# Optimization experiments

Hardware: AMD Instinct MI355X
Metric: run time of the kernel (lower is better)

Reference implementation:

```python
import jax, jax.numpy as jnp
import numpy as np

B, Q, K, A, H, C, O = 32, 512, 512, 256, 8, 32, 256  # batch, queries, keys, channels, heads, head_dim, out_dim


def setup_inputs() -> dict:
    key = jax.random.key(0)
    ks = jax.random.split(key, 12)
    s = 0.02
    return {
        "q_data": jax.random.normal(ks[0], (B, Q, A), jnp.float32),
        "m_data": jax.random.normal(ks[1], (B, K, A), jnp.float32),
        "bias": jax.random.normal(ks[2], (B, 1, 1, K), jnp.float32),
        "nonbatched_bias": jax.random.normal(ks[3], (H, Q, K), jnp.float32),
        "batched_bias": jax.random.normal(ks[4], (B, H, Q, K), jnp.float32),
        "query_w": jax.random.normal(ks[5], (A, H, C), jnp.float32) * s,
        "key_w": jax.random.normal(ks[6], (A, H, C), jnp.float32) * s,
        "value_w": jax.random.normal(ks[7], (A, H, C), jnp.float32) * s,
        "gating_w": jax.random.normal(ks[8], (A, H, C), jnp.float32) * s,
        "gating_b": jnp.ones((H, C), jnp.float32),
        "output_w": jax.random.normal(ks[9], (H, C, O), jnp.float32) * s,
        "output_b": jnp.zeros((O,), jnp.float32),
    }


def reference(q_data, m_data, bias, nonbatched_bias, batched_bias,
              query_w, key_w, value_w, gating_w, gating_b, output_w, output_b):
    key_scale = query_w.shape[-1] ** -0.5
    q = jnp.einsum('bqa,ahc->bqhc', q_data, query_w) * key_scale
    k = jnp.einsum('bka,ahc->bkhc', m_data, key_w)
    v = jnp.einsum('bka,ahc->bkhc', m_data, value_w)
    logits = jnp.einsum('bqhc,bkhc->bhqk', q, k) + bias
    logits = logits + nonbatched_bias[None] + batched_bias
    weights = jax.nn.softmax(logits, axis=-1)
    weighted_avg = jnp.einsum('bhqk,bkhc->bqhc', weights, v)
    gate = jax.nn.sigmoid(jnp.einsum('bqc,chv->bqhv', q_data, gating_w) + gating_b)
    weighted_avg = weighted_avg * gate
    return jnp.einsum('bqhc,hco->bqo', weighted_avg, output_w) + output_b
```

## Files before the change

### kernel.cpp

```cpp
#include <hip/hip_runtime.h>
#include <cstdint>
#include <cstddef>


typedef __attribute__((ext_vector_type(8))) short short8;
typedef __attribute__((ext_vector_type(4))) float f32x4;
typedef __attribute__((ext_vector_type(4))) unsigned int u32x4;
typedef __attribute__((ext_vector_type(2))) unsigned int u32x2;

#define DEVFN static __device__ __forceinline__
#define L2E 1.4426950408889634f

DEVFN float b2f(unsigned int bits16) {
  return __builtin_bit_cast(float, bits16 << 16);
}
DEVFN unsigned int pack2(float a, float b) {
  unsigned int r;
  asm("v_cvt_pk_bf16_f32 %0, %1, %2" : "=v"(r) : "v"(a), "v"(b));
  return r;
}
DEVFN f32x4 mfma16(short8 a, short8 b, f32x4 c) {
  return __builtin_amdgcn_mfma_f32_16x16x32_bf16(a, b, c, 0, 0, 0);
}

__global__ __launch_bounds__(256) void wtrans_kernel(
    const float* __restrict__ qw, const float* __restrict__ kw,
    const float* __restrict__ vw, const float* __restrict__ gw,
    const float* __restrict__ ow,
    unsigned short* __restrict__ wtq, unsigned short* __restrict__ wtk,
    unsigned short* __restrict__ wtv, unsigned short* __restrict__ wtg,
    unsigned short* __restrict__ wt3)
{
  const int matid = blockIdx.x >> 4;
  const int tile  = blockIdx.x & 15;
  const float* src = (matid == 0) ? qw : (matid == 1) ? kw : (matid == 2) ? vw
                   : (matid == 3) ? gw : ow;
  unsigned short* dst = (matid == 0) ? wtq : (matid == 1) ? wtk : (matid == 2) ? wtv
                      : (matid == 3) ? wtg : wt3;
  const int tr = (tile >> 2) * 64, tc = (tile & 3) * 64;
  __shared__ unsigned short T[64 * 72];
  const int t = threadIdx.x;
  {
    const int row = t >> 2, cb = (t & 3) * 16;
#pragma unroll
    for (int ii = 0; ii < 4; ++ii) {
      f32x4 v = *(const f32x4*)&src[(size_t)(tr + row) * 256 + tc + cb + ii * 4];
      u32x2 p; p.x = pack2(v.x, v.y); p.y = pack2(v.z, v.w);
      *(u32x2*)&T[row * 72 + cb + ii * 4] = p;
    }
  }
  __syncthreads();
  {
    const int c0 = t >> 2, rb = (t & 3) * 16;
    unsigned short vals[16];
#pragma unroll
    for (int m = 0; m < 16; ++m) vals[m] = T[(rb + m) * 72 + c0];
    u32x4 s0, s1;
    s0.x = (unsigned)vals[0]  | ((unsigned)vals[1]  << 16);
    s0.y = (unsigned)vals[2]  | ((unsigned)vals[3]  << 16);
    s0.z = (unsigned)vals[4]  | ((unsigned)vals[5]  << 16);
    s0.w = (unsigned)vals[6]  | ((unsigned)vals[7]  << 16);
    s1.x = (unsigned)vals[8]  | ((unsigned)vals[9]  << 16);
    s1.y = (unsigned)vals[10] | ((unsigned)vals[11] << 16);
    s1.z = (unsigned)vals[12] | ((unsigned)vals[13] << 16);
    s1.w = (unsigned)vals[14] | ((unsigned)vals[15] << 16);
    unsigned short* dp = &dst[(size_t)(tc + c0) * 256 + tr + rb];
    *(u32x4*)dp = s0;
    *(u32x4*)(dp + 8) = s1;
  }
}

__global__ __launch_bounds__(512, 4) void proj_kernel(
    const float* __restrict__ q_data, const float* __restrict__ m_data,
    const unsigned short* __restrict__ wtq, const unsigned short* __restrict__ wtk,
    const unsigned short* __restrict__ wtv, const unsigned short* __restrict__ wtg,
    const float* __restrict__ gating_b,
    unsigned short* __restrict__ qp, unsigned short* __restrict__ kp,
    unsigned short* __restrict__ vp, unsigned short* __restrict__ gate)
{
  const int bid = blockIdx.x;
  const bool mside = bid >= 256;
  const int r0 = (mside ? bid - 256 : bid) * 64;
  const float* inp = mside ? m_data : q_data;
  __shared__ unsigned short Alds[64 * 264];
  __shared__ unsigned short Wlds[2][256 * 40];
  const int t = threadIdx.x;
  const int lane = t & 63, wave = t >> 6;
  const int l15 = lane & 15, g = lane >> 4;
  const int stripe = wave & 3, nhalf = wave >> 2;

  {
    const int row = t >> 3, cb = (t & 7) * 32;
    const float* ip = &inp[(size_t)(r0 + row) * 256 + cb];
#pragma unroll
    for (int i = 0; i < 4; ++i) {
      f32x4 a0 = *(const f32x4*)&ip[i * 8];
      f32x4 a1 = *(const f32x4*)&ip[i * 8 + 4];
      u32x4 pk;
      pk.x = pack2(a0.x, a0.y); pk.y = pack2(a0.z, a0.w);
      pk.z = pack2(a1.x, a1.y); pk.w = pack2(a1.z, a1.w);
      *(u32x4*)&Alds[row * 264 + cb + i * 8] = pk;
    }
  }

  const unsigned short* wt0 = mside ? wtk : wtq;
  const unsigned short* wt1 = mside ? wtv : wtg;
  const int wrow = t & 255, whalf = t >> 8;

  {
    const u32x4* wsrc = (const u32x4*)&wt0[(size_t)wrow * 256 + whalf * 16];
    u32x4 a = wsrc[0], b = wsrc[1];
    *(u32x4*)&Wlds[0][wrow * 40 + whalf * 16 + 0] = a;
    *(u32x4*)&Wlds[0][wrow * 40 + whalf * 16 + 8] = b;
  }

  f32x4 acc[8];
#pragma unroll
  for (int j = 0; j < 8; ++j) acc[j] = f32x4{0.f, 0.f, 0.f, 0.f};

  const int arow = (stripe * 16 + l15) * 264 + 8 * g;
  const int grow = r0 + stripe * 16 + l15;
  const int ob = grow >> 9, oq = grow & 511;

#pragma unroll
  for (int s = 0; s < 16; ++s) {
    const int p = s & 1;
    __syncthreads();
    u32x4 nw0, nw1;
    if (s < 15) {
      const unsigned short* wt = (s + 1 < 8) ? wt0 : wt1;
      const u32x4* wsrc =
          (const u32x4*)&wt[(size_t)wrow * 256 + ((s + 1) & 7) * 32 + whalf * 16];
      nw0 = wsrc[0]; nw1 = wsrc[1];
    }
    const int ks = s & 7;
    short8 bf = __builtin_bit_cast(short8, *(const u32x4*)&Alds[arow + ks * 32]);
#pragma unroll
    for (int j = 0; j < 8; ++j) {
      short8 wf = __builtin_bit_cast(short8,
          *(const u32x4*)&Wlds[p][((nhalf * 8 + j) * 16 + l15) * 40 + 8 * g]);
      acc[j] = mfma16(wf, bf, acc[j]);
    }
    if (s < 15) {
      *(u32x4*)&Wlds[p ^ 1][wrow * 40 + whalf * 16 + 0] = nw0;
      *(u32x4*)&Wlds[p ^ 1][wrow * 40 + whalf * 16 + 8] = nw1;
    }
    if (s == 7 || s == 15) {
      const int oi = s >> 3;
      const float QS = 0.17677669529663687f * 1.4426950408889634f;
#pragma unroll
      for (int j = 0; j < 8; ++j) {
        const int n0 = (nhalf * 8 + j) * 16 + 4 * g;
        const int h = n0 >> 5, c0 = n0 & 31;
        const size_t idx = ((size_t)(ob * 8 + h) * 512 + oq) * 32 + c0;
        f32x4 v = acc[j];
        if (!mside) {
          if (oi == 0) {
            u32x2 st;
            st.x = pack2(v.x * QS, v.y * QS);
            st.y = pack2(v.z * QS, v.w * QS);
            *(u32x2*)&qp[idx] = st;
          } else {
            f32x4 gb = *(const f32x4*)&gating_b[n0];
            f32x4 gv;
            gv.x = 1.0f / (1.0f + exp2f(-(v.x + gb.x) * L2E));
            gv.y = 1.0f / (1.0f + exp2f(-(v.y + gb.y) * L2E));
            gv.z = 1.0f / (1.0f + exp2f(-(v.z + gb.z) * L2E));
            gv.w = 1.0f / (1.0f + exp2f(-(v.w + gb.w) * L2E));
            u32x2 st;
            st.x = pack2(gv.x, gv.y); st.y = pack2(gv.z, gv.w);
            *(u32x2*)&gate[idx] = st;
          }
        } else {
          u32x2 st;
          st.x = pack2(v.x, v.y); st.y = pack2(v.z, v.w);
          if (oi == 0) *(u32x2*)&kp[idx] = st;
          else         *(u32x2*)&vp[idx] = st;
        }
        acc[j] = f32x4{0.f, 0.f, 0.f, 0.f};
      }
    }
  }
}

__global__ __launch_bounds__(512, 4) void attn_kernel(
    const unsigned short* __restrict__ qp, const unsigned short* __restrict__ kp,
    const unsigned short* __restrict__ vp,
    const float* __restrict__ bias, const float* __restrict__ nbias,
    const float* __restrict__ bbias,
    unsigned short* __restrict__ wa)
{
  const int bid = blockIdx.x;
  const int h = bid & 7;
  const int qh = (bid >> 3) & 1;
  const int b = bid >> 4;
  const int bh = b * 8 + h;
  const int t = threadIdx.x;
  const int lane = t & 63, wave = t >> 6;
  const int l15 = lane & 15, g = lane >> 4;

  __shared__ unsigned short Klds[512 * 40];
  __shared__ unsigned short Vt[32 * 520];
  __shared__ float Bk[512];

  {
    const int row = t;
    const u32x4* ks = (const u32x4*)&kp[((size_t)bh * 512 + row) * 32];
    u32x4 k0 = ks[0], k1 = ks[1], k2 = ks[2], k3 = ks[3];
    *(u32x4*)&Klds[row * 40 + 0]  = k0;
    *(u32x4*)&Klds[row * 40 + 8]  = k1;
    *(u32x4*)&Klds[row * 40 + 16] = k2;
    *(u32x4*)&Klds[row * 40 + 24] = k3;
    const u32x4* vs = (const u32x4*)&vp[((size_t)bh * 512 + row) * 32];
#pragma unroll
    for (int cc = 0; cc < 4; ++cc) {
      u32x4 vv = vs[cc];
      unsigned int dw0 = vv.x, dw1 = vv.y, dw2 = vv.z, dw3 = vv.w;
      const int c = cc * 8;
      Vt[(c + 0) * 520 + row] = (unsigned short)(dw0 & 0xffff);
      Vt[(c + 1) * 520 + row] = (unsigned short)(dw0 >> 16);
      Vt[(c + 2) * 520 + row] = (unsigned short)(dw1 & 0xffff);
      Vt[(c + 3) * 520 + row] = (unsigned short)(dw1 >> 16);
      Vt[(c + 4) * 520 + row] = (unsigned short)(dw2 & 0xffff);
      Vt[(c + 5) * 520 + row] = (unsigned short)(dw2 >> 16);
      Vt[(c + 6) * 520 + row] = (unsigned short)(dw3 & 0xffff);
      Vt[(c + 7) * 520 + row] = (unsigned short)(dw3 >> 16);
    }
    if (t < 128) {
      f32x4 bv = *(const f32x4*)&bias[(size_t)b * 512 + t * 4];
      bv.x *= L2E; bv.y *= L2E; bv.z *= L2E; bv.w *= L2E;
      *(f32x4*)&Bk[t * 4] = bv;
    }
  }

  const int qbase = qh * 256 + wave * 32;
  short8 qf[2];
#pragma unroll
  for (int qt = 0; qt < 2; ++qt)
    qf[qt] = __builtin_bit_cast(short8,
        *(const u32x4*)&qp[((size_t)bh * 512 + qbase + qt * 16 + l15) * 32 + 8 * g]);

  const float* b0p = bbias + (size_t)bh * 512 * 512 + (size_t)(qbase + l15) * 512 + 4 * g;
  const float* b1p = b0p + 16 * 512;
  const float* n0p = nbias + (size_t)h * 512 * 512 + (size_t)(qbase + l15) * 512 + 4 * g;
  const float* n1p = n0p + 16 * 512;

  f32x4 acc[2][2];
#pragma unroll
  for (int ct = 0; ct < 2; ++ct)
#pragma unroll
    for (int qt = 0; qt < 2; ++qt) acc[ct][qt] = f32x4{0.f, 0.f, 0.f, 0.f};
  float l_part[2] = {0.f, 0.f};

  f32x4 Abb0 = *(const f32x4*)(b0p);
  f32x4 Abb1 = *(const f32x4*)(b0p + 16);
  f32x4 Anb0 = *(const f32x4*)(n0p);
  f32x4 Anb1 = *(const f32x4*)(n0p + 16);

  __syncthreads();

  const int pib = ((g & 1) << 4) | ((g >> 1) << 3);
  const bool godd = (g & 1) != 0;

  for (int kt = 0; kt < 16; ++kt) {
    const int k0 = kt * 32;
    short8 kf0 = __builtin_bit_cast(short8, *(const u32x4*)&Klds[(k0 + l15) * 40 + 8 * g]);
    short8 kf1 = __builtin_bit_cast(short8, *(const u32x4*)&Klds[(k0 + 16 + l15) * 40 + 8 * g]);
    short8 vf0 = __builtin_bit_cast(short8, *(const u32x4*)&Vt[l15 * 520 + k0 + pib]);
    short8 vf1 = __builtin_bit_cast(short8, *(const u32x4*)&Vt[(16 + l15) * 520 + k0 + pib]);
    f32x4 bks0 = *(const f32x4*)&Bk[k0 + 4 * g];
    f32x4 bks1 = *(const f32x4*)&Bk[k0 + 16 + 4 * g];
    f32x4 Bbb0 = *(const f32x4*)(b1p + k0);
    f32x4 Bbb1 = *(const f32x4*)(b1p + k0 + 16);
    f32x4 Bnb0 = *(const f32x4*)(n1p + k0);
    f32x4 Bnb1 = *(const f32x4*)(n1p + k0 + 16);

#pragma unroll
    for (int qt = 0; qt < 2; ++qt) {
      f32x4 bb0, bb1, nb0, nb1;
      if (qt == 0) { bb0 = Abb0; bb1 = Abb1; nb0 = Anb0; nb1 = Anb1; }
      else         { bb0 = Bbb0; bb1 = Bbb1; nb0 = Bnb0; nb1 = Bnb1; }
      f32x4 c0 = bb0 * L2E + (nb0 * L2E + bks0);
      f32x4 c1 = bb1 * L2E + (nb1 * L2E + bks1);
      f32x4 s0 = mfma16(kf0, qf[qt], c0);
      f32x4 s1 = mfma16(kf1, qf[qt], c1);
      if (qt == 0 && kt < 15) {
        Abb0 = *(const f32x4*)(b0p + k0 + 32);
        Abb1 = *(const f32x4*)(b0p + k0 + 48);
        Anb0 = *(const f32x4*)(n0p + k0 + 32);
        Anb1 = *(const f32x4*)(n0p + k0 + 48);
      }
      f32x4 p0, p1;
      p0.x = exp2f(s0.x); p0.y = exp2f(s0.y);
      p0.z = exp2f(s0.z); p0.w = exp2f(s0.w);
      p1.x = exp2f(s1.x); p1.y = exp2f(s1.y);
      p1.z = exp2f(s1.z); p1.w = exp2f(s1.w);
      l_part[qt] += ((p0.x + p0.y) + (p0.z + p0.w)) +
                    ((p1.x + p1.y) + (p1.z + p1.w));
      unsigned int d0 = pack2(p0.x, p0.y), d1 = pack2(p0.z, p0.w);
      unsigned int e0 = pack2(p1.x, p1.y), e1 = pack2(p1.z, p1.w);
      unsigned int pd0 = __shfl_xor(d0, 16, 64), pd1 = __shfl_xor(d1, 16, 64);
      unsigned int pe0 = __shfl_xor(e0, 16, 64), pe1 = __shfl_xor(e1, 16, 64);
      u32x4 pfu;
      pfu.x = godd ? pe0 : d0;
      pfu.y = godd ? pe1 : d1;
      pfu.z = godd ? e0 : pd0;
      pfu.w = godd ? e1 : pd1;
      short8 pf = __builtin_bit_cast(short8, pfu);
      acc[0][qt] = mfma16(vf0, pf, acc[0][qt]);
      acc[1][qt] = mfma16(vf1, pf, acc[1][qt]);
    }
  }

  unsigned short* wab = wa + (size_t)bh * 512 * 32;
#pragma unroll
  for (int qt = 0; qt < 2; ++qt) {
    float l = l_part[qt];
    l += __shfl_xor(l, 16, 64);
    l += __shfl_xor(l, 32, 64);
    const float rl = 1.0f / l;
    const int q = qbase + qt * 16 + l15;
#pragma unroll
    for (int ct = 0; ct < 2; ++ct) {
      f32x4 v = acc[ct][qt];
      u32x2 st;
      st.x = pack2(v.x * rl, v.y * rl);
      st.y = pack2(v.z * rl, v.w * rl);
      *(u32x2*)&wab[q * 32 + ct * 16 + 4 * g] = st;
    }
  }
}

__global__ __launch_bounds__(256, 2) void outp_kernel(
    const unsigned short* __restrict__ wa, const unsigned short* __restrict__ gate,
    const unsigned short* __restrict__ wt3, const float* __restrict__ out_b,
    float* __restrict__ out)
{
  const int r0 = blockIdx.x * 32;
  const int t = threadIdx.x;
  const int lane = t & 63, wave = t >> 6;
  const int l15 = lane & 15, g = lane >> 4;
  const int stripe = wave & 1, half = wave >> 1;
  __shared__ unsigned short Wlds[2][256 * 40];

  const int grow = r0 + stripe * 16 + l15;
  const int b = grow >> 9, q = grow & 511;

  {
    const u32x4* wsrc = (const u32x4*)&wt3[(size_t)t * 256];
    u32x4 a = wsrc[0], bb = wsrc[1], c = wsrc[2], d = wsrc[3];
    *(u32x4*)&Wlds[0][t * 40 + 0]  = a;
    *(u32x4*)&Wlds[0][t * 40 + 8]  = bb;
    *(u32x4*)&Wlds[0][t * 40 + 16] = c;
    *(u32x4*)&Wlds[0][t * 40 + 24] = d;
  }
  size_t aidx = ((size_t)(b * 8 + 0) * 512 + q) * 32 + 8 * g;
  u32x4 cwv = *(const u32x4*)&wa[aidx];
  u32x4 cgv = *(const u32x4*)&gate[aidx];

  f32x4 acc[8];
#pragma unroll
  for (int j = 0; j < 8; ++j) acc[j] = f32x4{0.f, 0.f, 0.f, 0.f};

#pragma unroll
  for (int s = 0; s < 8; ++s) {
    const int p = s & 1;
    __syncthreads();
    u32x4 nw0, nw1, nw2, nw3, nwv, ngv;
    if (s < 7) {
      const u32x4* wsrc = (const u32x4*)&wt3[(size_t)t * 256 + (s + 1) * 32];
      nw0 = wsrc[0]; nw1 = wsrc[1]; nw2 = wsrc[2]; nw3 = wsrc[3];
      const size_t na = ((size_t)(b * 8 + s + 1) * 512 + q) * 32 + 8 * g;
      nwv = *(const u32x4*)&wa[na];
      ngv = *(const u32x4*)&gate[na];
    }
    float f0 = b2f(cwv.x & 0xffff) * b2f(cgv.x & 0xffff);
    float f1 = b2f(cwv.x >> 16)    * b2f(cgv.x >> 16);
    float f2 = b2f(cwv.y & 0xffff) * b2f(cgv.y & 0xffff);
    float f3 = b2f(cwv.y >> 16)    * b2f(cgv.y >> 16);
    float f4 = b2f(cwv.z & 0xffff) * b2f(cgv.z & 0xffff);
    float f5 = b2f(cwv.z >> 16)    * b2f(cgv.z >> 16);
    float f6 = b2f(cwv.w & 0xffff) * b2f(cgv.w & 0xffff);
    float f7 = b2f(cwv.w >> 16)    * b2f(cgv.w >> 16);
    u32x4 au;
    au.x = pack2(f0, f1); au.y = pack2(f2, f3);
    au.z = pack2(f4, f5); au.w = pack2(f6, f7);
    short8 af = __builtin_bit_cast(short8, au);
#pragma unroll
    for (int j = 0; j < 8; ++j) {
      short8 wf = __builtin_bit_cast(short8,
          *(const u32x4*)&Wlds[p][((half * 8 + j) * 16 + l15) * 40 + 8 * g]);
      acc[j] = mfma16(wf, af, acc[j]);
    }
    if (s < 7) {
      *(u32x4*)&Wlds[p ^ 1][t * 40 + 0]  = nw0;
      *(u32x4*)&Wlds[p ^ 1][t * 40 + 8]  = nw1;
      *(u32x4*)&Wlds[p ^ 1][t * 40 + 16] = nw2;
      *(u32x4*)&Wlds[p ^ 1][t * 40 + 24] = nw3;
      cwv = nwv; cgv = ngv;
    }
  }
#pragma unroll
  for (int j = 0; j < 8; ++j) {
    const int o0 = (half * 8 + j) * 16 + 4 * g;
    f32x4 ob4 = *(const f32x4*)&out_b[o0];
    f32x4 v = acc[j] + ob4;
    *(f32x4*)&out[(size_t)grow * 256 + o0] = v;
  }
}

extern "C" void kernel_launch(void* const* d_in, const int* in_sizes, int n_in,
                              void* d_out, int out_size, void* d_ws, size_t ws_size,
                              hipStream_t stream)
{
  const float* q_data   = (const float*)d_in[0];
  const float* m_data   = (const float*)d_in[1];
  const float* bias     = (const float*)d_in[2];
  const float* nbb      = (const float*)d_in[3];
  const float* bbb      = (const float*)d_in[4];
  const float* query_w  = (const float*)d_in[5];
  const float* key_w    = (const float*)d_in[6];
  const float* value_w  = (const float*)d_in[7];
  const float* gating_w = (const float*)d_in[8];
  const float* gating_b = (const float*)d_in[9];
  const float* output_w = (const float*)d_in[10];
  const float* output_b = (const float*)d_in[11];
  float* out = (float*)d_out;

  const size_t QP_B   = (size_t)32 * 8 * 512 * 32 * 2;
  const size_t GATE_B = (size_t)32 * 8 * 512 * 32 * 2;
  const size_t WT_B   = (size_t)256 * 256 * 2;

  char* ws = (char*)d_ws;
  unsigned short* qp  = (unsigned short*)(ws);
  unsigned short* kp  = (unsigned short*)(ws + QP_B);
  unsigned short* vp  = (unsigned short*)(ws + 2 * QP_B);
  unsigned short* wab = (unsigned short*)(ws + 3 * QP_B);
  unsigned short* gat = (unsigned short*)(ws + 4 * QP_B);
  unsigned short* wtq = (unsigned short*)(ws + 4 * QP_B + GATE_B);
  unsigned short* wtk = (unsigned short*)(ws + 4 * QP_B + GATE_B + WT_B);
  unsigned short* wtv = (unsigned short*)(ws + 4 * QP_B + GATE_B + 2 * WT_B);
  unsigned short* wtg = (unsigned short*)(ws + 4 * QP_B + GATE_B + 3 * WT_B);
  unsigned short* wt3 = (unsigned short*)(ws + 4 * QP_B + GATE_B + 4 * WT_B);
  const size_t need = 4 * QP_B + GATE_B + 5 * WT_B;
  if (ws_size < need) return;

  hipLaunchKernelGGL(wtrans_kernel, dim3(80), dim3(256), 0, stream,
                     query_w, key_w, value_w, gating_w, output_w,
                     wtq, wtk, wtv, wtg, wt3);
  hipLaunchKernelGGL(proj_kernel, dim3(512), dim3(512), 0, stream,
                     q_data, m_data, wtq, wtk, wtv, wtg, gating_b,
                     qp, kp, vp, gat);
  hipLaunchKernelGGL(attn_kernel, dim3(512), dim3(512), 0, stream,
                     qp, kp, vp, bias, nbb, bbb, wab);
  hipLaunchKernelGGL(outp_kernel, dim3(512), dim3(256), 0, stream,
                     wab, gat, wt3, output_b, out);
}
```

Measured before the change: 133.0 us.

## Write V transposed from projection kernel and stream K/V fragments from global

The projection kernel now computes the V pass with swapped MFMA operands and stores V in a [b,h,c,k] transposed layout. The attention kernel drops its K/V LDS staging and scalar V transpose, and instead loads K and V MFMA fragments directly from global memory, prefetching one key tile ahead in registers. This removes LDS traffic, the transpose stores and 36KB of shared memory per block, which could raise occupancy. The cost is that each wave now reads K/V from global/L2 on its own rather than sharing one copy through LDS, and the transposed V store pattern is less coalesced.

```diff
diff --git a/kernel.cpp b/kernel.cpp
--- a/kernel.cpp
+++ b/kernel.cpp
@@ -121,6 +121,8 @@
   const int arow = (stripe * 16 + l15) * 264 + 8 * g;
   const int grow = r0 + stripe * 16 + l15;
   const int ob = grow >> 9, oq = grow & 511;
+  const int growv = r0 + stripe * 16 + 4 * g;
+  const int obv = growv >> 9, okv = growv & 511;
 
 #pragma unroll
   for (int s = 0; s < 16; ++s) {
@@ -135,11 +137,13 @@
     }
     const int ks = s & 7;
     short8 bf = __builtin_bit_cast(short8, *(const u32x4*)&Alds[arow + ks * 32]);
+    const bool vpass = mside && (s >= 8);
 #pragma unroll
     for (int j = 0; j < 8; ++j) {
       short8 wf = __builtin_bit_cast(short8,
           *(const u32x4*)&Wlds[p][((nhalf * 8 + j) * 16 + l15) * 40 + 8 * g]);
-      acc[j] = mfma16(wf, bf, acc[j]);
+      if (vpass) acc[j] = mfma16(bf, wf, acc[j]);
+      else       acc[j] = mfma16(wf, bf, acc[j]);
     }
     if (s < 15) {
       *(u32x4*)&Wlds[p ^ 1][wrow * 40 + whalf * 16 + 0] = nw0;
@@ -150,11 +154,11 @@
       const float QS = 0.17677669529663687f * 1.4426950408889634f;
 #pragma unroll
       for (int j = 0; j < 8; ++j) {
-        const int n0 = (nhalf * 8 + j) * 16 + 4 * g;
-        const int h = n0 >> 5, c0 = n0 & 31;
-        const size_t idx = ((size_t)(ob * 8 + h) * 512 + oq) * 32 + c0;
         f32x4 v = acc[j];
         if (!mside) {
+          const int n0 = (nhalf * 8 + j) * 16 + 4 * g;
+          const int h = n0 >> 5, c0 = n0 & 31;
+          const size_t idx = ((size_t)(ob * 8 + h) * 512 + oq) * 32 + c0;
           if (oi == 0) {
             u32x2 st;
             st.x = pack2(v.x * QS, v.y * QS);
@@ -171,11 +175,20 @@
             st.x = pack2(gv.x, gv.y); st.y = pack2(gv.z, gv.w);
             *(u32x2*)&gate[idx] = st;
           }
-        } else {
+        } else if (oi == 0) {
+          const int n0 = (nhalf * 8 + j) * 16 + 4 * g;
+          const int h = n0 >> 5, c0 = n0 & 31;
+          const size_t idx = ((size_t)(ob * 8 + h) * 512 + oq) * 32 + c0;
           u32x2 st;
           st.x = pack2(v.x, v.y); st.y = pack2(v.z, v.w);
-          if (oi == 0) *(u32x2*)&kp[idx] = st;
-          else         *(u32x2*)&vp[idx] = st;
+          *(u32x2*)&kp[idx] = st;
+        } else {
+          const int nv = (nhalf * 8 + j) * 16 + l15;
+          const int hv = nv >> 5, cv = nv & 31;
+          const size_t idx = ((size_t)(obv * 8 + hv) * 32 + cv) * 512 + okv;
+          u32x2 st;
+          st.x = pack2(v.x, v.y); st.y = pack2(v.z, v.w);
+          *(u32x2*)&vp[idx] = st;
         }
         acc[j] = f32x4{0.f, 0.f, 0.f, 0.f};
       }
@@ -199,38 +212,12 @@
   const int lane = t & 63, wave = t >> 6;
   const int l15 = lane & 15, g = lane >> 4;
 
-  __shared__ unsigned short Klds[512 * 40];
-  __shared__ unsigned short Vt[32 * 520];
   __shared__ float Bk[512];
 
-  {
-    const int row = t;
-    const u32x4* ks = (const u32x4*)&kp[((size_t)bh * 512 + row) * 32];
-    u32x4 k0 = ks[0], k1 = ks[1], k2 = ks[2], k3 = ks[3];
-    *(u32x4*)&Klds[row * 40 + 0]  = k0;
-    *(u32x4*)&Klds[row * 40 + 8]  = k1;
-    *(u32x4*)&Klds[row * 40 + 16] = k2;
-    *(u32x4*)&Klds[row * 40 + 24] = k3;
-    const u32x4* vs = (const u32x4*)&vp[((size_t)bh * 512 + row) * 32];
-#pragma unroll
-    for (int cc = 0; cc < 4; ++cc) {
-      u32x4 vv = vs[cc];
-      unsigned int dw0 = vv.x, dw1 = vv.y, dw2 = vv.z, dw3 = vv.w;
-      const int c = cc * 8;
-      Vt[(c + 0) * 520 + row] = (unsigned short)(dw0 & 0xffff);
-      Vt[(c + 1) * 520 + row] = (unsigned short)(dw0 >> 16);
-      Vt[(c + 2) * 520 + row] = (unsigned short)(dw1 & 0xffff);
-      Vt[(c + 3) * 520 + row] = (unsigned short)(dw1 >> 16);
-      Vt[(c + 4) * 520 + row] = (unsigned short)(dw2 & 0xffff);
-      Vt[(c + 5) * 520 + row] = (unsigned short)(dw2 >> 16);
-      Vt[(c + 6) * 520 + row] = (unsigned short)(dw3 & 0xffff);
-      Vt[(c + 7) * 520 + row] = (unsigned short)(dw3 >> 16);
-    }
-    if (t < 128) {
-      f32x4 bv = *(const f32x4*)&bias[(size_t)b * 512 + t * 4];
-      bv.x *= L2E; bv.y *= L2E; bv.z *= L2E; bv.w *= L2E;
-      *(f32x4*)&Bk[t * 4] = bv;
-    }
+  if (t < 128) {
+    f32x4 bv = *(const f32x4*)&bias[(size_t)b * 512 + t * 4];
+    bv.x *= L2E; bv.y *= L2E; bv.z *= L2E; bv.w *= L2E;
+    *(f32x4*)&Bk[t * 4] = bv;
   }
 
   const int qbase = qh * 256 + wave * 32;
@@ -239,6 +226,14 @@
   for (int qt = 0; qt < 2; ++qt)
     qf[qt] = __builtin_bit_cast(short8,
         *(const u32x4*)&qp[((size_t)bh * 512 + qbase + qt * 16 + l15) * 32 + 8 * g]);
+
+  const int pib = ((g & 1) << 4) | ((g >> 1) << 3);
+  const bool godd = (g & 1) != 0;
+
+  const unsigned short* kf0p = kp + (size_t)bh * 512 * 32 + (size_t)l15 * 32 + 8 * g;
+  const unsigned short* kf1p = kf0p + 16 * 32;
+  const unsigned short* vf0p = vp + (size_t)bh * 32 * 512 + (size_t)l15 * 512 + pib;
+  const unsigned short* vf1p = vf0p + 16 * 512;
 
   const float* b0p = bbias + (size_t)bh * 512 * 512 + (size_t)(qbase + l15) * 512 + 4 * g;
   const float* b1p = b0p + 16 * 512;
@@ -252,6 +247,10 @@
     for (int qt = 0; qt < 2; ++qt) acc[ct][qt] = f32x4{0.f, 0.f, 0.f, 0.f};
   float l_part[2] = {0.f, 0.f};
 
+  u32x4 kf0n = *(const u32x4*)(kf0p);
+  u32x4 kf1n = *(const u32x4*)(kf1p);
+  u32x4 vf0n = *(const u32x4*)(vf0p);
+  u32x4 vf1n = *(const u32x4*)(vf1p);
   f32x4 Abb0 = *(const f32x4*)(b0p);
   f32x4 Abb1 = *(const f32x4*)(b0p + 16);
   f32x4 Anb0 = *(const f32x4*)(n0p);
@@ -259,15 +258,18 @@
 
   __syncthreads();
 
-  const int pib = ((g & 1) << 4) | ((g >> 1) << 3);
-  const bool godd = (g & 1) != 0;
-
   for (int kt = 0; kt < 16; ++kt) {
     const int k0 = kt * 32;
-    short8 kf0 = __builtin_bit_cast(short8, *(const u32x4*)&Klds[(k0 + l15) * 40 + 8 * g]);
-    short8 kf1 = __builtin_bit_cast(short8, *(const u32x4*)&Klds[(k0 + 16 + l15) * 40 + 8 * g]);
-    short8 vf0 = __builtin_bit_cast(short8, *(const u32x4*)&Vt[l15 * 520 + k0 + pib]);
-    short8 vf1 = __builtin_bit_cast(short8, *(const u32x4*)&Vt[(16 + l15) * 520 + k0 + pib]);
+    short8 kf0 = __builtin_bit_cast(short8, kf0n);
+    short8 kf1 = __builtin_bit_cast(short8, kf1n);
+    short8 vf0 = __builtin_bit_cast(short8, vf0n);
+    short8 vf1 = __builtin_bit_cast(short8, vf1n);
+    if (kt < 15) {
+      kf0n = *(const u32x4*)(kf0p + (k0 + 32) * 32);
+      kf1n = *(const u32x4*)(kf1p + (k0 + 32) * 32);
+      vf0n = *(const u32x4*)(vf0p + k0 + 32);
+      vf1n = *(const u32x4*)(vf1p + k0 + 32);
+    }
     f32x4 bks0 = *(const f32x4*)&Bk[k0 + 4 * g];
     f32x4 bks1 = *(const f32x4*)&Bk[k0 + 16 + 4 * g];
     f32x4 Bbb0 = *(const f32x4*)(b1p + k0);
```

After: 156.6 us. 1.18x slower.

## Stream batched bias through LDS with async global_load_lds double buffering

Applied to the files above, without the earlier changes.

The batched bias tile, the largest HBM stream, is now loaded with direct global-to-LDS async loads into a swizzled double buffer two k-steps ahead. Waits use explicit vmcnt counters, and the nonbatched bias register prefetch is restructured to match. Occupancy is lowered from 4 to 2 blocks per CU in the launch bounds to fit the extra 64KB of LDS. The aim is better latency hiding and coalescing on the bias read, at the cost of fewer resident waves and fragile manual waitcnt handling.

```diff
diff --git a/kernel.cpp b/kernel.cpp
--- a/kernel.cpp
+++ b/kernel.cpp
@@ -22,6 +22,10 @@
 DEVFN f32x4 mfma16(short8 a, short8 b, f32x4 c) {
   return __builtin_amdgcn_mfma_f32_16x16x32_bf16(a, b, c, 0, 0, 0);
 }
+#define GLOAD_LDS16(gp, lp)                                        \
+  __builtin_amdgcn_global_load_lds(                                \
+      (const __attribute__((address_space(1))) void*)(gp),         \
+      (__attribute__((address_space(3))) void*)(lp), 16, 0, 0)
 
 __global__ __launch_bounds__(256) void wtrans_kernel(
     const float* __restrict__ qw, const float* __restrict__ kw,
@@ -183,7 +187,7 @@
   }
 }
 
-__global__ __launch_bounds__(512, 4) void attn_kernel(
+__global__ __launch_bounds__(512, 2) void attn_kernel(
     const unsigned short* __restrict__ qp, const unsigned short* __restrict__ kp,
     const unsigned short* __restrict__ vp,
     const float* __restrict__ bias, const float* __restrict__ nbias,
@@ -201,6 +205,7 @@
 
   __shared__ unsigned short Klds[512 * 40];
   __shared__ unsigned short Vt[32 * 520];
+  __shared__ float Bb[2][8192];
   __shared__ float Bk[512];
 
   {
@@ -240,9 +245,12 @@
     qf[qt] = __builtin_bit_cast(short8,
         *(const u32x4*)&qp[((size_t)bh * 512 + qbase + qt * 16 + l15) * 32 + 8 * g]);
 
-  const float* b0p = bbias + (size_t)bh * 512 * 512 + (size_t)(qbase + l15) * 512 + 4 * g;
-  const float* b1p = b0p + 16 * 512;
-  const float* n0p = nbias + (size_t)h * 512 * 512 + (size_t)(qbase + l15) * 512 + 4 * g;
+  const float* bbb_blk = bbias + (size_t)bh * 262144 + (size_t)(qh * 256) * 512;
+  const int qc = lane >> 3, sl = lane & 7;
+  const float* wsrc0 = bbb_blk + (size_t)(wave * 32) * 512
+                     + (size_t)qc * 512 + ((sl ^ qc) << 2);
+
+  const float* n0p = nbias + (size_t)h * 262144 + (size_t)(qbase + l15) * 512 + 4 * g;
   const float* n1p = n0p + 16 * 512;
 
   f32x4 acc[2][2];
@@ -252,17 +260,28 @@
     for (int qt = 0; qt < 2; ++qt) acc[ct][qt] = f32x4{0.f, 0.f, 0.f, 0.f};
   float l_part[2] = {0.f, 0.f};
 
-  f32x4 Abb0 = *(const f32x4*)(b0p);
-  f32x4 Abb1 = *(const f32x4*)(b0p + 16);
-  f32x4 Anb0 = *(const f32x4*)(n0p);
-  f32x4 Anb1 = *(const f32x4*)(n0p + 16);
+#pragma unroll
+  for (int i = 0; i < 4; ++i)
+    GLOAD_LDS16(wsrc0 + (size_t)i * 4096, &Bb[0][(wave * 4 + i) * 256]);
+#pragma unroll
+  for (int i = 0; i < 4; ++i)
+    GLOAD_LDS16(wsrc0 + (size_t)i * 4096 + 32, &Bb[1][(wave * 4 + i) * 256]);
+  f32x4 Cn00 = *(const f32x4*)(n0p);
+  f32x4 Cn01 = *(const f32x4*)(n0p + 16);
+  f32x4 Cn10 = *(const f32x4*)(n1p);
+  f32x4 Cn11 = *(const f32x4*)(n1p + 16);
 
   __syncthreads();
 
   const int pib = ((g & 1) << 4) | ((g >> 1) << 3);
   const bool godd = (g & 1) != 0;
+  const int sw0 = (g ^ (l15 & 7)) << 2;
+  const int sw1 = ((g + 4) ^ (l15 & 7)) << 2;
+  const int bq0 = (wave * 32 + l15) * 32;
+  const int bq1 = bq0 + 16 * 32;
 
   for (int kt = 0; kt < 16; ++kt) {
+    const int p = kt & 1;
     const int k0 = kt * 32;
     short8 kf0 = __builtin_bit_cast(short8, *(const u32x4*)&Klds[(k0 + l15) * 40 + 8 * g]);
     short8 kf1 = __builtin_bit_cast(short8, *(const u32x4*)&Klds[(k0 + 16 + l15) * 40 + 8 * g]);
@@ -270,26 +289,22 @@
     short8 vf1 = __builtin_bit_cast(short8, *(const u32x4*)&Vt[(16 + l15) * 520 + k0 + pib]);
     f32x4 bks0 = *(const f32x4*)&Bk[k0 + 4 * g];
     f32x4 bks1 = *(const f32x4*)&Bk[k0 + 16 + 4 * g];
-    f32x4 Bbb0 = *(const f32x4*)(b1p + k0);
-    f32x4 Bbb1 = *(const f32x4*)(b1p + k0 + 16);
-    f32x4 Bnb0 = *(const f32x4*)(n1p + k0);
-    f32x4 Bnb1 = *(const f32x4*)(n1p + k0 + 16);
+    const float* bp = Bb[p];
+    f32x4 bb00 = *(const f32x4*)&bp[bq0 + sw0];
+    f32x4 bb01 = *(const f32x4*)&bp[bq0 + sw1];
+    f32x4 bb10 = *(const f32x4*)&bp[bq1 + sw0];
+    f32x4 bb11 = *(const f32x4*)&bp[bq1 + sw1];
 
 #pragma unroll
     for (int qt = 0; qt < 2; ++qt) {
-      f32x4 bb0, bb1, nb0, nb1;
-      if (qt == 0) { bb0 = Abb0; bb1 = Abb1; nb0 = Anb0; nb1 = Anb1; }
-      else         { bb0 = Bbb0; bb1 = Bbb1; nb0 = Bnb0; nb1 = Bnb1; }
+      f32x4 bb0 = qt ? bb10 : bb00;
+      f32x4 bb1 = qt ? bb11 : bb01;
+      f32x4 nb0 = qt ? Cn10 : Cn00;
+      f32x4 nb1 = qt ? Cn11 : Cn01;
       f32x4 c0 = bb0 * L2E + (nb0 * L2E + bks0);
       f32x4 c1 = bb1 * L2E + (nb1 * L2E + bks1);
       f32x4 s0 = mfma16(kf0, qf[qt], c0);
       f32x4 s1 = mfma16(kf1, qf[qt], c1);
-      if (qt == 0 && kt < 15) {
-        Abb0 = *(const f32x4*)(b0p + k0 + 32);
-        Abb1 = *(const f32x4*)(b0p + k0 + 48);
-        Anb0 = *(const f32x4*)(n0p + k0 + 32);
-        Anb1 = *(const f32x4*)(n0p + k0 + 48);
-      }
       f32x4 p0, p1;
       p0.x = exp2f(s0.x); p0.y = exp2f(s0.y);
       p0.z = exp2f(s0.z); p0.w = exp2f(s0.w);
@@ -310,6 +325,22 @@
       acc[0][qt] = mfma16(vf0, pf, acc[0][qt]);
       acc[1][qt] = mfma16(vf1, pf, acc[1][qt]);
     }
+
+    asm volatile("" ::: "memory");
+    if (kt < 14) {
+      const float* ws = wsrc0 + (size_t)(kt + 2) * 32;
+#pragma unroll
+      for (int i = 0; i < 4; ++i)
+        GLOAD_LDS16(ws + (size_t)i * 4096, &Bb[p][(wave * 4 + i) * 256]);
+    }
+    if (kt < 15) {
+      Cn00 = *(const f32x4*)(n0p + k0 + 32);
+      Cn01 = *(const f32x4*)(n0p + k0 + 48);
+      Cn10 = *(const f32x4*)(n1p + k0 + 32);
+      Cn11 = *(const f32x4*)(n1p + k0 + 48);
+    }
+    if (kt < 14)       asm volatile("s_waitcnt vmcnt(8)" ::: "memory");
+    else if (kt == 14) asm volatile("s_waitcnt vmcnt(4)" ::: "memory");
   }
 
   unsigned short* wab = wa + (size_t)bh * 512 * 32;
```

Result: faster. 122.3 us (-8.0%).
